# Kernel tuning notes

Hardware: AMD Instinct MI355X
Metric: run time of the kernel (lower is better)

Reference implementation:

```python
import jax, jax.numpy as jnp
import numpy as np


def setup_inputs() -> dict:
    key = jax.random.key(0)
    x = jax.random.normal(key, (8, 2048, 512), dtype=jnp.float32)
    return {"x": x}


def reference(x):
    # x: [B, S, D]; unscaled causal self-attention with Q=K=V=x
    B, S, D = x.shape
    scores = jnp.einsum('bsd,btd->bst', x, x)  # [B, S, S]
    causal = jnp.tril(jnp.ones((S, S), dtype=bool))  # True where allowed
    scores = jnp.where(causal[None, :, :], scores, -jnp.inf)
    attn = jax.nn.softmax(scores, axis=-1)
    out = jnp.einsum('bst,btd->bsd', attn, x)  # [B, S, D]
    return out
```

## Files before the change

### kernel.cpp

```cpp
#include <hip/hip_runtime.h>


#define S_LEN 2048
#define D_DIM 512
#define BATCH_ELEMS 1048576

typedef short s16x8 __attribute__((ext_vector_type(8)));
typedef float f32x4 __attribute__((ext_vector_type(4)));

__device__ __forceinline__ unsigned short f2b_rne(float f) {
  unsigned int u = __float_as_uint(f);
  return (unsigned short)((u + 0x7FFFu + ((u >> 16) & 1u)) >> 16);
}
__device__ __forceinline__ unsigned short f2b_fast(float f) {
  return (unsigned short)((__float_as_uint(f) + 0x8000u) >> 16);
}

template <int CTRL>
__device__ __forceinline__ float dppf(float x) {
  return __uint_as_float((unsigned)__builtin_amdgcn_update_dpp(
      0, (int)__float_as_uint(x), CTRL, 0xF, 0xF, true));
}
__device__ __forceinline__ float red16_max(float v) {
  v = fmaxf(v, dppf<0xB1>(v));
  v = fmaxf(v, dppf<0x4E>(v));
  v = fmaxf(v, dppf<0x124>(v));
  v = fmaxf(v, dppf<0x128>(v));
  return v;
}
__device__ __forceinline__ float red16_sum(float v) {
  v += dppf<0xB1>(v);
  v += dppf<0x4E>(v);
  v += dppf<0x124>(v);
  v += dppf<0x128>(v);
  return v;
}

__global__ void pack_kernel(const float* __restrict__ x,
                            unsigned short* __restrict__ Kf,
                            unsigned short* __restrict__ Vf) {
  __shared__ unsigned short A[64 * 72];
  __shared__ unsigned short T[64 * 72];
  const int bid = blockIdx.x;
  const int b = bid >> 8, rem = bid & 255;
  const int s0 = (rem >> 3) * 64, d0 = (rem & 7) * 64;
  const int tid = threadIdx.x;

  #pragma unroll
  for (int it = 0; it < 2; ++it) {
    int slot = it * 256 + tid;
    int row = slot >> 3, c = slot & 7;
    const float* src = x + ((size_t)(b * S_LEN + s0 + row)) * D_DIM + d0 + c * 8;
    const float4 v0 = *(const float4*)(src);
    const float4 v1 = *(const float4*)(src + 4);
    s16x8 o;
    o[0] = (short)f2b_rne(v0.x); o[1] = (short)f2b_rne(v0.y);
    o[2] = (short)f2b_rne(v0.z); o[3] = (short)f2b_rne(v0.w);
    o[4] = (short)f2b_rne(v1.x); o[5] = (short)f2b_rne(v1.y);
    o[6] = (short)f2b_rne(v1.z); o[7] = (short)f2b_rne(v1.w);
    *(s16x8*)&A[row * 72 + c * 8] = o;
  }
  __syncthreads();

  {
    int sr = tid >> 4, sc = tid & 15;
    ushort4 a0 = *(const ushort4*)&A[(4 * sr + 0) * 72 + 4 * sc];
    ushort4 a1 = *(const ushort4*)&A[(4 * sr + 1) * 72 + 4 * sc];
    ushort4 a2 = *(const ushort4*)&A[(4 * sr + 2) * 72 + 4 * sc];
    ushort4 a3 = *(const ushort4*)&A[(4 * sr + 3) * 72 + 4 * sc];
    ushort4 t0; t0.x = a0.x; t0.y = a1.x; t0.z = a2.x; t0.w = a3.x;
    ushort4 t1; t1.x = a0.y; t1.y = a1.y; t1.z = a2.y; t1.w = a3.y;
    ushort4 t2; t2.x = a0.z; t2.y = a1.z; t2.z = a2.z; t2.w = a3.z;
    ushort4 t3; t3.x = a0.w; t3.y = a1.w; t3.z = a2.w; t3.w = a3.w;
    *(ushort4*)&T[(4 * sc + 0) * 72 + 4 * sr] = t0;
    *(ushort4*)&T[(4 * sc + 1) * 72 + 4 * sr] = t1;
    *(ushort4*)&T[(4 * sc + 2) * 72 + 4 * sr] = t2;
    *(ushort4*)&T[(4 * sc + 3) * 72 + 4 * sr] = t3;
  }
  __syncthreads();

  #pragma unroll
  for (int it = 0; it < 2; ++it) {
    int slot = it * 256 + tid;
    int frag = slot >> 6;
    int lane = slot & 63;
    int l15 = lane & 15, quad = lane >> 4;
    int f1 = frag >> 1, f0 = frag & 1;
    {
      s16x8 val = *(const s16x8*)&A[(f1 * 16 + l15) * 72 + f0 * 32 + quad * 8];
      size_t kg = (size_t)(s0 >> 4) + f1, db = (size_t)(d0 >> 5) + f0;
      *(s16x8*)(Kf + (size_t)b * BATCH_ELEMS + (kg * 16 + db) * 512 + lane * 8) = val;
    }
    {
      s16x8 val = *(const s16x8*)&T[(f1 * 16 + l15) * 72 + f0 * 32 + quad * 8];
      size_t dg = (size_t)(d0 >> 4) + f1, kb = (size_t)(s0 >> 5) + f0;
      *(s16x8*)(Vf + (size_t)b * BATCH_ELEMS + (dg * 64 + kb) * 512 + lane * 8) = val;
    }
  }
}

__global__ __launch_bounds__(256, 2)
void attn_kernel(const unsigned short* __restrict__ Kf,
                 const unsigned short* __restrict__ Vf,
                 float* __restrict__ out) {
  __shared__ unsigned short ldsK[16384];
  __shared__ float Xc[4][512];
  __shared__ unsigned short Pw[4][16 * 40];

  const int bid = blockIdx.x;
  const int bat = bid & 7;
  const int rg = 127 - (bid >> 3);
  const int q0 = rg * 16;
  const int tmax = rg >> 1;
  const int tid = threadIdx.x;
  const int w = tid >> 6;
  const int lane = tid & 63;
  const int l15 = lane & 15, quad = lane >> 4;
  const size_t batOff = (size_t)bat * BATCH_ELEMS;

  auto stageK = [&](int kt) {
    const unsigned short* ks =
        Kf + batOff + (size_t)kt * 16384 + (size_t)(w * 8) * 512 + lane * 8;
    #pragma unroll
    for (int i = 0; i < 8; ++i) {
      __builtin_amdgcn_global_load_lds(
          (const __attribute__((address_space(1))) unsigned int*)(ks + i * 512),
          (__attribute__((address_space(3))) unsigned int*)&ldsK[(w * 8 + i) * 512],
          16, 0, 0);
    }
  };

  s16x8 vreg[8];
  auto loadV = [&](int kt) {
    const unsigned short* vb = Vf + batOff + (size_t)kt * 512 + lane * 8;
    #pragma unroll
    for (int dgl = 0; dgl < 8; ++dgl)
      vreg[dgl] = *(const s16x8*)(vb + (size_t)(w * 8 + dgl) * 32768);
  };

  stageK(0);
  loadV(0);

  s16x8 qf[4];
  {
    const unsigned short* qb =
        Kf + batOff + ((size_t)rg * 16 + w * 4) * 512 + lane * 8;
    #pragma unroll
    for (int i = 0; i < 4; ++i) qf[i] = *(const s16x8*)(qb + i * 512);
  }

  f32x4 O[8];
  float m[4], l[4];
  #pragma unroll
  for (int n = 0; n < 8; ++n) O[n] = (f32x4){0.f, 0.f, 0.f, 0.f};
  #pragma unroll
  for (int r = 0; r < 4; ++r) { m[r] = -3e38f; l[r] = 0.f; }

  __syncthreads();

  for (int kt = 0;; ++kt) {
    f32x4 sacc[2];
    sacc[0] = (f32x4){0.f, 0.f, 0.f, 0.f};
    sacc[1] = (f32x4){0.f, 0.f, 0.f, 0.f};
    __builtin_amdgcn_s_setprio(1);
    #pragma unroll
    for (int i = 0; i < 4; ++i) {
      int db = w * 4 + i;
      s16x8 k0 = *(const s16x8*)&ldsK[db * 512 + lane * 8];
      s16x8 k1 = *(const s16x8*)&ldsK[(16 + db) * 512 + lane * 8];
      sacc[0] = __builtin_amdgcn_mfma_f32_16x16x32_bf16(qf[i], k0, sacc[0], 0, 0, 0);
      sacc[1] = __builtin_amdgcn_mfma_f32_16x16x32_bf16(qf[i], k1, sacc[1], 0, 0, 0);
    }
    __builtin_amdgcn_s_setprio(0);

    *(f32x4*)&Xc[w][lane * 4] = sacc[0];
    *(f32x4*)&Xc[w][256 + lane * 4] = sacc[1];
    asm volatile("s_waitcnt lgkmcnt(0)" ::: "memory");
    __builtin_amdgcn_s_barrier();
    __builtin_amdgcn_sched_barrier(0);
    {
      f32x4 s0 = *(const f32x4*)&Xc[0][lane * 4];
      s0 += *(const f32x4*)&Xc[1][lane * 4];
      s0 += *(const f32x4*)&Xc[2][lane * 4];
      s0 += *(const f32x4*)&Xc[3][lane * 4];
      f32x4 s1 = *(const f32x4*)&Xc[0][256 + lane * 4];
      s1 += *(const f32x4*)&Xc[1][256 + lane * 4];
      s1 += *(const f32x4*)&Xc[2][256 + lane * 4];
      s1 += *(const f32x4*)&Xc[3][256 + lane * 4];
      sacc[0] = s0;
      sacc[1] = s1;
    }

    if (kt < tmax) stageK(kt + 1);

    if (kt == tmax) {
      #pragma unroll
      for (int kg2 = 0; kg2 < 2; ++kg2)
        #pragma unroll
        for (int r = 0; r < 4; ++r) {
          int key = kt * 32 + kg2 * 16 + l15;
          int row = q0 + quad * 4 + r;
          if (key > row) sacc[kg2][r] = -3e38f;
        }
    }

    float mt[4], alpha[4];
    #pragma unroll
    for (int r = 0; r < 4; ++r)
      mt[r] = red16_max(fmaxf(sacc[0][r], sacc[1][r]));
    bool needAny = (mt[0] > m[0]) | (mt[1] > m[1]) | (mt[2] > m[2]) | (mt[3] > m[3]);
    unsigned long long bal = __ballot(needAny);
    if (bal) {
      #pragma unroll
      for (int r = 0; r < 4; ++r) {
        float mn = fmaxf(m[r], mt[r]);
        alpha[r] = __expf(m[r] - mn);
        m[r] = mn;
      }
    } else {
      #pragma unroll
      for (int r = 0; r < 4; ++r) alpha[r] = 1.0f;
    }
    float p[2][4];
    #pragma unroll
    for (int kg2 = 0; kg2 < 2; ++kg2)
      #pragma unroll
      for (int r = 0; r < 4; ++r) p[kg2][r] = __expf(sacc[kg2][r] - m[r]);
    #pragma unroll
    for (int r = 0; r < 4; ++r)
      l[r] = l[r] * alpha[r] + red16_sum(p[0][r] + p[1][r]);

    #pragma unroll
    for (int kg2 = 0; kg2 < 2; ++kg2)
      #pragma unroll
      for (int r = 0; r < 4; ++r)
        Pw[w][(quad * 4 + r) * 40 + kg2 * 16 + l15] = f2b_fast(p[kg2][r]);
    s16x8 pa = *(const s16x8*)&Pw[w][l15 * 40 + quad * 8];

    if (bal) {
      #pragma unroll
      for (int n = 0; n < 8; ++n)
        #pragma unroll
        for (int r = 0; r < 4; ++r) O[n][r] *= alpha[r];
    }

    __builtin_amdgcn_s_setprio(1);
    #pragma unroll
    for (int dgl = 0; dgl < 8; ++dgl)
      O[dgl] = __builtin_amdgcn_mfma_f32_16x16x32_bf16(pa, vreg[dgl], O[dgl], 0, 0, 0);
    __builtin_amdgcn_s_setprio(0);

    if (kt == tmax) break;

    loadV(kt + 1);

    asm volatile("s_waitcnt vmcnt(8)" ::: "memory");
    __builtin_amdgcn_s_barrier();
    __builtin_amdgcn_sched_barrier(0);
  }

  float invl[4];
  #pragma unroll
  for (int r = 0; r < 4; ++r) invl[r] = 1.0f / l[r];
  float* ob = out + ((size_t)(bat * S_LEN + q0)) * D_DIM + w * 128;
  #pragma unroll
  for (int dgl = 0; dgl < 8; ++dgl)
    #pragma unroll
    for (int r = 0; r < 4; ++r)
      ob[(size_t)(quad * 4 + r) * D_DIM + dgl * 16 + l15] = O[dgl][r] * invl[r];
}

extern "C" void kernel_launch(void* const* d_in, const int* in_sizes, int n_in,
                              void* d_out, int out_size, void* d_ws, size_t ws_size,
                              hipStream_t stream) {
  (void)in_sizes; (void)n_in; (void)out_size; (void)ws_size;
  const float* x = (const float*)d_in[0];
  float* out = (float*)d_out;
  unsigned short* Kf = (unsigned short*)d_ws;
  unsigned short* Vf = (unsigned short*)((char*)d_ws + (16u << 20));
  pack_kernel<<<2048, 256, 0, stream>>>(x, Kf, Vf);
  attn_kernel<<<1024, 256, 0, stream>>>(Kf, Vf, out);
}
```

Measured before the change: 180.5 us.

## Load K fragments directly into registers and double-buffer score reduction buffer

Measured after the change: 170.3 us. -5.6%, faster.

```diff
diff --git a/kernel.cpp b/kernel.cpp
--- a/kernel.cpp
+++ b/kernel.cpp
@@ -103,8 +103,7 @@
 void attn_kernel(const unsigned short* __restrict__ Kf,
                  const unsigned short* __restrict__ Vf,
                  float* __restrict__ out) {
-  __shared__ unsigned short ldsK[16384];
-  __shared__ float Xc[4][512];
+  __shared__ float Xc[2][4][512];
   __shared__ unsigned short Pw[4][16 * 40];
 
   const int bid = blockIdx.x;
@@ -118,15 +117,13 @@
   const int l15 = lane & 15, quad = lane >> 4;
   const size_t batOff = (size_t)bat * BATCH_ELEMS;
 
-  auto stageK = [&](int kt) {
-    const unsigned short* ks =
-        Kf + batOff + (size_t)kt * 16384 + (size_t)(w * 8) * 512 + lane * 8;
-    #pragma unroll
-    for (int i = 0; i < 8; ++i) {
-      __builtin_amdgcn_global_load_lds(
-          (const __attribute__((address_space(1))) unsigned int*)(ks + i * 512),
-          (__attribute__((address_space(3))) unsigned int*)&ldsK[(w * 8 + i) * 512],
-          16, 0, 0);
+  s16x8 kreg[8];
+  auto loadK = [&](int kt) {
+    const unsigned short* kb = Kf + batOff + (size_t)kt * 16384 + lane * 8;
+    #pragma unroll
+    for (int i = 0; i < 4; ++i) {
+      kreg[i]     = *(const s16x8*)(kb + (size_t)(w * 4 + i) * 512);
+      kreg[4 + i] = *(const s16x8*)(kb + (size_t)(16 + w * 4 + i) * 512);
     }
   };
 
@@ -138,7 +135,7 @@
       vreg[dgl] = *(const s16x8*)(vb + (size_t)(w * 8 + dgl) * 32768);
   };
 
-  stageK(0);
+  loadK(0);
   loadV(0);
 
   s16x8 qf[4];
@@ -156,42 +153,39 @@
   #pragma unroll
   for (int r = 0; r < 4; ++r) { m[r] = -3e38f; l[r] = 0.f; }
 
-  __syncthreads();
-
   for (int kt = 0;; ++kt) {
+    const int p = kt & 1;
+
     f32x4 sacc[2];
     sacc[0] = (f32x4){0.f, 0.f, 0.f, 0.f};
     sacc[1] = (f32x4){0.f, 0.f, 0.f, 0.f};
     __builtin_amdgcn_s_setprio(1);
     #pragma unroll
     for (int i = 0; i < 4; ++i) {
-      int db = w * 4 + i;
-      s16x8 k0 = *(const s16x8*)&ldsK[db * 512 + lane * 8];
-      s16x8 k1 = *(const s16x8*)&ldsK[(16 + db) * 512 + lane * 8];
-      sacc[0] = __builtin_amdgcn_mfma_f32_16x16x32_bf16(qf[i], k0, sacc[0], 0, 0, 0);
-      sacc[1] = __builtin_amdgcn_mfma_f32_16x16x32_bf16(qf[i], k1, sacc[1], 0, 0, 0);
+      sacc[0] = __builtin_amdgcn_mfma_f32_16x16x32_bf16(qf[i], kreg[i], sacc[0], 0, 0, 0);
+      sacc[1] = __builtin_amdgcn_mfma_f32_16x16x32_bf16(qf[i], kreg[4 + i], sacc[1], 0, 0, 0);
     }
     __builtin_amdgcn_s_setprio(0);
 
-    *(f32x4*)&Xc[w][lane * 4] = sacc[0];
-    *(f32x4*)&Xc[w][256 + lane * 4] = sacc[1];
+    if (kt < tmax) loadK(kt + 1);
+
+    *(f32x4*)&Xc[p][w][lane * 4] = sacc[0];
+    *(f32x4*)&Xc[p][w][256 + lane * 4] = sacc[1];
     asm volatile("s_waitcnt lgkmcnt(0)" ::: "memory");
     __builtin_amdgcn_s_barrier();
     __builtin_amdgcn_sched_barrier(0);
     {
-      f32x4 s0 = *(const f32x4*)&Xc[0][lane * 4];
-      s0 += *(const f32x4*)&Xc[1][lane * 4];
-      s0 += *(const f32x4*)&Xc[2][lane * 4];
-      s0 += *(const f32x4*)&Xc[3][lane * 4];
-      f32x4 s1 = *(const f32x4*)&Xc[0][256 + lane * 4];
-      s1 += *(const f32x4*)&Xc[1][256 + lane * 4];
-      s1 += *(const f32x4*)&Xc[2][256 + lane * 4];
-      s1 += *(const f32x4*)&Xc[3][256 + lane * 4];
+      f32x4 s0 = *(const f32x4*)&Xc[p][0][lane * 4];
+      s0 += *(const f32x4*)&Xc[p][1][lane * 4];
+      s0 += *(const f32x4*)&Xc[p][2][lane * 4];
+      s0 += *(const f32x4*)&Xc[p][3][lane * 4];
+      f32x4 s1 = *(const f32x4*)&Xc[p][0][256 + lane * 4];
+      s1 += *(const f32x4*)&Xc[p][1][256 + lane * 4];
+      s1 += *(const f32x4*)&Xc[p][2][256 + lane * 4];
+      s1 += *(const f32x4*)&Xc[p][3][256 + lane * 4];
       sacc[0] = s0;
       sacc[1] = s1;
     }
-
-    if (kt < tmax) stageK(kt + 1);
 
     if (kt == tmax) {
       #pragma unroll
@@ -221,20 +215,20 @@
       #pragma unroll
       for (int r = 0; r < 4; ++r) alpha[r] = 1.0f;
     }
-    float p[2][4];
+    float p2[2][4];
     #pragma unroll
     for (int kg2 = 0; kg2 < 2; ++kg2)
       #pragma unroll
-      for (int r = 0; r < 4; ++r) p[kg2][r] = __expf(sacc[kg2][r] - m[r]);
+      for (int r = 0; r < 4; ++r) p2[kg2][r] = __expf(sacc[kg2][r] - m[r]);
     #pragma unroll
     for (int r = 0; r < 4; ++r)
-      l[r] = l[r] * alpha[r] + red16_sum(p[0][r] + p[1][r]);
+      l[r] = l[r] * alpha[r] + red16_sum(p2[0][r] + p2[1][r]);
 
     #pragma unroll
     for (int kg2 = 0; kg2 < 2; ++kg2)
       #pragma unroll
       for (int r = 0; r < 4; ++r)
-        Pw[w][(quad * 4 + r) * 40 + kg2 * 16 + l15] = f2b_fast(p[kg2][r]);
+        Pw[w][(quad * 4 + r) * 40 + kg2 * 16 + l15] = f2b_fast(p2[kg2][r]);
     s16x8 pa = *(const s16x8*)&Pw[w][l15 * 40 + quad * 8];
 
     if (bal) {
@@ -253,10 +247,6 @@
     if (kt == tmax) break;
 
     loadV(kt + 1);
-
-    asm volatile("s_waitcnt vmcnt(8)" ::: "memory");
-    __builtin_amdgcn_s_barrier();
-    __builtin_amdgcn_sched_barrier(0);
   }
 
   float invl[4];
```
